# Kernel tuning notes

Measured on AMD Instinct MI355X. Metric: run time of the kernel, lower is better.

## Reference

```python
import jax, jax.numpy as jnp
import numpy as np

SEQ, B, I, H = 512, 64, 1024, 1024

def setup_inputs() -> dict:
    key = jax.random.key(0)
    ks = jax.random.split(key, 6)
    scale_ih = 1.0 / np.sqrt(I)
    scale_hh = 1.0 / np.sqrt(H)
    return {
        "input": jax.random.normal(ks[0], (SEQ, B, I), dtype=jnp.float32),
        "h_0": jax.random.normal(ks[1], (1, B, H), dtype=jnp.float32),
        "weight_ih": jax.random.normal(ks[2], (3 * H, I), dtype=jnp.float32) * scale_ih,
        "weight_hh": jax.random.normal(ks[3], (3 * H, H), dtype=jnp.float32) * scale_hh,
        "bias_ih": jax.random.normal(ks[4], (3 * H,), dtype=jnp.float32) * scale_hh,
        "bias_hh": jax.random.normal(ks[5], (3 * H,), dtype=jnp.float32) * scale_hh,
    }


def _gru_lbr0(input, h0, weight_ih, weight_hh, bias_ih, bias_hh):
    """Unidirectional GRU, ONNX linear_before_reset=0 semantics.

    r_t = sigmoid(x W_ir^T + b_ir + h W_hr^T + b_hr)
    z_t = sigmoid(x W_iz^T + b_iz + h W_hz^T + b_hz)
    n_t = tanh(x W_in^T + b_in + (r_t * h) W_hn^T + b_hn)
    h_t = (1 - z_t) * n_t + z_t * h
    """
    hidden = h0.shape[-1]
    # Precompute all input projections in one big GEMM: (S, B, 3H)
    gx = jnp.einsum('sbi,gi->sbg', input, weight_ih) + bias_ih
    W_hr, W_hz, W_hn = jnp.split(weight_hh, 3, axis=0)
    b_hr, b_hz, b_hn = jnp.split(bias_hh, 3, axis=0)

    def step(h, gx_t):
        gx_r, gx_z, gx_n = jnp.split(gx_t, 3, axis=-1)
        r = jax.nn.sigmoid(gx_r + h @ W_hr.T + b_hr)
        z = jax.nn.sigmoid(gx_z + h @ W_hz.T + b_hz)
        n = jnp.tanh(gx_n + (r * h) @ W_hn.T + b_hn)
        h_new = (1.0 - z) * n + z * h
        return h_new, h_new

    h_n, outputs = jax.lax.scan(step, h0, gx)
    return outputs, h_n  # (S, B, H), (B, H)


def reference(input, h_0, weight_ih, weight_hh, bias_ih, bias_hh):
    seq_len, batch, _ = input.shape
    hidden = weight_hh.shape[1]
    outputs, h_n = _gru_lbr0(input, h_0[0], weight_ih, weight_hh, bias_ih, bias_hh)
    # Match GRUWrapper output layout: Y = (S, num_dir=1, B, H), Y_h = (1, B, H)
    Y = outputs.reshape(seq_len, batch, 1, hidden).transpose(0, 2, 1, 3)
    Y_h = h_n[None, :, :]
    return (Y, Y_h)
```

## Files before the change

### kernel.cpp

```cpp
#include <hip/hip_runtime.h>

typedef unsigned short ushort_t;
typedef short sh8 __attribute__((ext_vector_type(8)));
typedef float f32x4 __attribute__((ext_vector_type(4)));

#define MFMA16(a,b,c) __builtin_amdgcn_mfma_f32_16x16x32_bf16((a),(b),(c),0,0,0)

#define SEQL   512
#define BATCH  64
#define HDIM   1024
#define G3     3072
#define AROWS  (SEQL*BATCH)
#define YSZ    (SEQL*BATCH*HDIM)
#define BH     (BATCH*HDIM)
#define NWG    64

__device__ __forceinline__ ushort_t f2bf(float x) {
  unsigned u = __float_as_uint(x);
  u += 0x7FFFu + ((u >> 16) & 1u);
  return (ushort_t)(u >> 16);
}
__device__ __forceinline__ float bf2f(ushort_t h) {
  return __uint_as_float(((unsigned)h) << 16);
}

__global__ void cvt_kernel(const float* __restrict__ wih, const float* __restrict__ h0,
                           ushort_t* __restrict__ WihH, ushort_t* __restrict__ WihL,
                           ushort_t* __restrict__ hH) {
  const int NW = G3 * HDIM;
  int i0 = blockIdx.x * blockDim.x + threadIdx.x;
  int stride = gridDim.x * blockDim.x;
  for (int i = i0; i < NW; i += stride) {
    float x = wih[i]; ushort_t h = f2bf(x);
    WihH[i] = h; WihL[i] = f2bf(x - bf2f(h));
  }
  for (int i = i0; i < BH; i += stride) {
    hH[i] = f2bf(h0[i]);
  }
}

__global__ __launch_bounds__(256) void gemm_gx(
    const float* __restrict__ A,
    const ushort_t* __restrict__ BHp, const ushort_t* __restrict__ BLp,
    const float* __restrict__ bias,
    float* __restrict__ gx)
{
  int bid = blockIdx.x;
  int mt = bid / 12, ntp = bid % 12;
  int w = threadIdx.x >> 6, l = threadIdx.x & 63;
  int lr = l & 15, lk = (l >> 4) * 8;

  f32x4 acc[2][2][8];
  #pragma unroll
  for (int n2 = 0; n2 < 2; ++n2)
    #pragma unroll
    for (int mi = 0; mi < 2; ++mi)
      #pragma unroll
      for (int ni = 0; ni < 8; ++ni) acc[n2][mi][ni] = (f32x4){0.f, 0.f, 0.f, 0.f};

  int arow0 = mt * 128 + w * 32 + lr;
  int brow0 = ntp * 256 + lr;

  for (int k0 = 0; k0 < HDIM; k0 += 32) {
    int ka = k0 + lk;
    sh8 aH[2], aL[2];
    #pragma unroll
    for (int mi = 0; mi < 2; ++mi) {
      const float* ap = A + (size_t)(arow0 + mi * 16) * HDIM + ka;
      float4 x0 = *(const float4*)ap;
      float4 x1 = *(const float4*)(ap + 4);
      float xs[8] = {x0.x, x0.y, x0.z, x0.w, x1.x, x1.y, x1.z, x1.w};
      #pragma unroll
      for (int j = 0; j < 8; ++j) {
        ushort_t h = f2bf(xs[j]);
        aH[mi][j] = (short)h;
        aL[mi][j] = (short)f2bf(xs[j] - bf2f(h));
      }
    }
    #pragma unroll
    for (int n2 = 0; n2 < 2; ++n2) {
      #pragma unroll
      for (int ni = 0; ni < 8; ++ni) {
        int brow = brow0 + n2 * 128 + ni * 16;
        const ushort_t* bh = BHp + (size_t)brow * HDIM + ka;
        const ushort_t* bl = BLp + (size_t)brow * HDIM + ka;
        sh8 bHf = *(const sh8*)bh;
        sh8 bLf = *(const sh8*)bl;
        #pragma unroll
        for (int mi = 0; mi < 2; ++mi) {
          acc[n2][mi][ni] = MFMA16(aH[mi], bHf, acc[n2][mi][ni]);
          acc[n2][mi][ni] = MFMA16(aH[mi], bLf, acc[n2][mi][ni]);
          acc[n2][mi][ni] = MFMA16(aL[mi], bHf, acc[n2][mi][ni]);
        }
      }
    }
  }
  int rb = (l >> 4) * 4;
  #pragma unroll
  for (int n2 = 0; n2 < 2; ++n2)
    #pragma unroll
    for (int mi = 0; mi < 2; ++mi)
      #pragma unroll
      for (int ni = 0; ni < 8; ++ni) {
        int col = ntp * 256 + n2 * 128 + ni * 16 + lr;
        float b = bias[col];
        #pragma unroll
        for (int j = 0; j < 4; ++j) {
          int row = mt * 128 + w * 32 + mi * 16 + rb + j;
          __builtin_nontemporal_store(acc[n2][mi][ni][j] + b, &gx[(size_t)row * G3 + col]);
        }
      }
}

__device__ __forceinline__ void gbar_flat(unsigned* slots, int g, int tid, unsigned e) {
  __syncthreads();
  if (tid < 64) {
    if (tid == 0)
      __hip_atomic_store(slots + g * 32, e, __ATOMIC_RELEASE, __HIP_MEMORY_SCOPE_AGENT);
    unsigned* sp = slots + tid * 32;
    while (__hip_atomic_load(sp, __ATOMIC_RELAXED, __HIP_MEMORY_SCOPE_AGENT) < e)
      __builtin_amdgcn_s_sleep(1);
    (void)__hip_atomic_load(sp, __ATOMIC_ACQUIRE, __HIP_MEMORY_SCOPE_AGENT);
  }
  __syncthreads();
}

__global__ __launch_bounds__(256, 1) void gru_rec(
    const float* __restrict__ gx,
    const float* __restrict__ whh,
    const float* __restrict__ bhh,
    const float* __restrict__ h0f,
    ushort_t* __restrict__ hH,
    ushort_t* __restrict__ rhH,
    float* __restrict__ Y, float* __restrict__ Yh,
    unsigned* __restrict__ slots)
{
  extern __shared__ char lds[];
  const int g = blockIdx.x;
  const int tid = threadIdx.x;
  const int w = tid >> 6, l = tid & 63;
  const int lr = l & 15, lk = (l >> 4) * 8, rb = (l >> 4) * 4;
  const int c0 = g * 16, m0 = w * 16;
  const int c = c0 + lr;

  #pragma unroll
  for (int p = 0; p < 32; ++p) {
    int q = tid + p * 256;
    int flat = q * 16;
    int lrow = flat >> 11;
    int off = flat & 2047;
    int dst = flat ^ ((lrow & 7) << 4);
    int col = off >> 1;
    const float* src;
    bool lo = false;
    if (lrow < 16)      src = whh + (size_t)(c0 + lrow) * HDIM + col;
    else if (lrow < 32) src = whh + (size_t)(1024 + c0 + lrow - 16) * HDIM + col;
    else if (lrow < 48) src = whh + (size_t)(2048 + c0 + lrow - 32) * HDIM + col;
    else              { src = whh + (size_t)(2048 + c0 + lrow - 48) * HDIM + col; lo = true; }
    float4 x0 = *(const float4*)src;
    float4 x1 = *(const float4*)(src + 4);
    float xs[8] = {x0.x, x0.y, x0.z, x0.w, x1.x, x1.y, x1.z, x1.w};
    union { ushort_t v[8]; sh8 s; } pk;
    #pragma unroll
    for (int j = 0; j < 8; ++j) {
      ushort_t hi = f2bf(xs[j]);
      pk.v[j] = lo ? f2bf(xs[j] - bf2f(hi)) : hi;
    }
    *(sh8*)(lds + dst) = pk.s;
  }
  __syncthreads();

  const float br = bhh[c], bz = bhh[1024 + c], bn = bhh[2048 + c];
  unsigned bar = 0;

  float hold[4];
  #pragma unroll
  for (int j = 0; j < 4; ++j) hold[j] = h0f[(m0 + rb + j) * HDIM + c];

  float gxr[4], gxz[4], gxn[4];
  #pragma unroll
  for (int j = 0; j < 4; ++j) {
    int b = m0 + rb + j;
    gxr[j] = __builtin_nontemporal_load(gx + (size_t)b * G3 + c);
    gxz[j] = __builtin_nontemporal_load(gx + (size_t)b * G3 + 1024 + c);
    gxn[j] = __builtin_nontemporal_load(gx + (size_t)b * G3 + 2048 + c);
  }

  for (int t = 0; t < SEQL; ++t) {
    const int par = t & 1;

    const ushort_t* ha = hH + par * BH + (size_t)(m0 + lr) * HDIM + lk;
    sh8 bufa[32];
    #pragma unroll
    for (int i = 0; i < 32; ++i) bufa[i] = *(const sh8*)(ha + i * 32);

    f32x4 accR = (f32x4){0,0,0,0}, accZ = (f32x4){0,0,0,0};
    #pragma unroll
    for (int i = 0; i < 32; ++i) {
      int byt = ((lr << 11) + ((i * 32 + lk) << 1)) ^ ((lr & 7) << 4);
      sh8 rW = *(const sh8*)(lds + byt);
      sh8 zW = *(const sh8*)(lds + 32768 + byt);
      accR = MFMA16(bufa[i], rW, accR);
      accZ = MFMA16(bufa[i], zW, accZ);
    }

    float zreg[4];
    #pragma unroll
    for (int j = 0; j < 4; ++j) {
      int b = m0 + rb + j;
      float pr = accR[j] + gxr[j] + br;
      float pz = accZ[j] + gxz[j] + bz;
      float r = 1.f / (1.f + __expf(-pr));
      zreg[j] = 1.f / (1.f + __expf(-pz));
      rhH[b * HDIM + c] = f2bf(r * hold[j]);
    }
    ++bar;
    gbar_flat(slots, g, tid, bar);

    const ushort_t* ra = rhH + (size_t)(m0 + lr) * HDIM + lk;
    #pragma unroll
    for (int i = 0; i < 32; ++i) bufa[i] = *(const sh8*)(ra + i * 32);

    int tn = (t + 1 < SEQL) ? t + 1 : t;
    {
      const float* gxn2 = gx + (size_t)tn * (BATCH * G3);
      #pragma unroll
      for (int j = 0; j < 4; ++j) {
        int b = m0 + rb + j;
        gxr[j] = __builtin_nontemporal_load(gxn2 + (size_t)b * G3 + c);
        gxz[j] = __builtin_nontemporal_load(gxn2 + (size_t)b * G3 + 1024 + c);
      }
    }

    f32x4 accN = (f32x4){0,0,0,0};
    #pragma unroll
    for (int i = 0; i < 32; ++i) {
      int byt = ((lr << 11) + ((i * 32 + lk) << 1)) ^ ((lr & 7) << 4);
      sh8 nW = *(const sh8*)(lds + 65536 + byt);
      sh8 nLo = *(const sh8*)(lds + 98304 + byt);
      accN = MFMA16(bufa[i], nW, accN);
      accN = MFMA16(bufa[i], nLo, accN);
    }

    ushort_t* hHn = hH + (par ^ 1) * BH;
    float gxnN[4];
    {
      const float* gxn2 = gx + (size_t)tn * (BATCH * G3);
      #pragma unroll
      for (int j = 0; j < 4; ++j) {
        int b = m0 + rb + j;
        gxnN[j] = __builtin_nontemporal_load(gxn2 + (size_t)b * G3 + 2048 + c);
      }
    }
    #pragma unroll
    for (int j = 0; j < 4; ++j) {
      int b = m0 + rb + j;
      float pn = accN[j] + gxn[j] + bn;
      float n = tanhf(pn);
      float z = zreg[j];
      float hnew = (1.f - z) * n + z * hold[j];
      hold[j] = hnew;
      __builtin_nontemporal_store(hnew, &Y[(size_t)t * BH + b * HDIM + c]);
      hHn[b * HDIM + c] = f2bf(hnew);
      if (t == SEQL - 1) __builtin_nontemporal_store(hnew, &Yh[b * HDIM + c]);
    }
    #pragma unroll
    for (int j = 0; j < 4; ++j) gxn[j] = gxnN[j];

    if (t < SEQL - 1) {
      ++bar;
      gbar_flat(slots, g, tid, bar);
    }
  }
}

extern "C" void kernel_launch(void* const* d_in, const int* in_sizes, int n_in,
                              void* d_out, int out_size, void* d_ws, size_t ws_size,
                              hipStream_t stream) {
  const float* input = (const float*)d_in[0];
  const float* h0    = (const float*)d_in[1];
  const float* wih   = (const float*)d_in[2];
  const float* whh   = (const float*)d_in[3];
  const float* bih   = (const float*)d_in[4];
  const float* bhh   = (const float*)d_in[5];

  char* ws = (char*)d_ws;
  size_t o = 0;
  float* gx = (float*)(ws + o);         o += (size_t)AROWS * G3 * 4;
  ushort_t* WihH = (ushort_t*)(ws + o); o += (size_t)G3 * HDIM * 2;
  ushort_t* WihL = (ushort_t*)(ws + o); o += (size_t)G3 * HDIM * 2;
  ushort_t* hH = (ushort_t*)(ws + o);   o += 2 * (size_t)BH * 2;
  ushort_t* rhH = (ushort_t*)(ws + o);  o += (size_t)BH * 2;
  unsigned* slots = (unsigned*)(ws + o); o += (size_t)NWG * 128;

  float* Y  = (float*)d_out;
  float* Yh = (float*)d_out + (size_t)YSZ;

  (void)hipFuncSetAttribute((const void*)gru_rec,
                            hipFuncAttributeMaxDynamicSharedMemorySize, 131072);

  (void)hipMemsetAsync(slots, 0, (size_t)NWG * 128, stream);
  cvt_kernel<<<2048, 256, 0, stream>>>(wih, h0, WihH, WihL, hH);
  gemm_gx<<<(AROWS / 128) * (G3 / 256), 256, 0, stream>>>(input, WihH, WihL, bih, gx);
  gru_rec<<<64, 256, 131072, stream>>>(gx, whh, bhh, h0, hH, rhH, Y, Yh, slots);
}
```

Before: 9.163 ms.

## Drop low-part activation MFMA and halve N tile in input-projection GEMM

Removes the aL (activation low-bf16) split so the input-projection GEMM does 2 MFMAs per tile instead of 3, skipping the xL*WH term. It also shrinks each block's N tile from 256 to 128 columns, doubling the grid and cutting accumulator registers. Fewer registers may raise occupancy, but the A tile is now converted twice as often across blocks. Accuracy drops because the input's low-order bits are lost, leaving only bf16 precision on x.

```diff
diff --git a/kernel.cpp b/kernel.cpp
--- a/kernel.cpp
+++ b/kernel.cpp
@@ -46,24 +46,22 @@
     float* __restrict__ gx)
 {
   int bid = blockIdx.x;
-  int mt = bid / 12, ntp = bid % 12;
+  int mt = bid / 24, nt = bid % 24;
   int w = threadIdx.x >> 6, l = threadIdx.x & 63;
   int lr = l & 15, lk = (l >> 4) * 8;
 
-  f32x4 acc[2][2][8];
-  #pragma unroll
-  for (int n2 = 0; n2 < 2; ++n2)
-    #pragma unroll
-    for (int mi = 0; mi < 2; ++mi)
-      #pragma unroll
-      for (int ni = 0; ni < 8; ++ni) acc[n2][mi][ni] = (f32x4){0.f, 0.f, 0.f, 0.f};
+  f32x4 acc[2][8];
+  #pragma unroll
+  for (int mi = 0; mi < 2; ++mi)
+    #pragma unroll
+    for (int ni = 0; ni < 8; ++ni) acc[mi][ni] = (f32x4){0.f, 0.f, 0.f, 0.f};
 
   int arow0 = mt * 128 + w * 32 + lr;
-  int brow0 = ntp * 256 + lr;
+  int brow0 = nt * 128 + lr;
 
   for (int k0 = 0; k0 < HDIM; k0 += 32) {
     int ka = k0 + lk;
-    sh8 aH[2], aL[2];
+    sh8 aH[2];
     #pragma unroll
     for (int mi = 0; mi < 2; ++mi) {
       const float* ap = A + (size_t)(arow0 + mi * 16) * HDIM + ka;
@@ -71,45 +69,34 @@
       float4 x1 = *(const float4*)(ap + 4);
       float xs[8] = {x0.x, x0.y, x0.z, x0.w, x1.x, x1.y, x1.z, x1.w};
       #pragma unroll
-      for (int j = 0; j < 8; ++j) {
-        ushort_t h = f2bf(xs[j]);
-        aH[mi][j] = (short)h;
-        aL[mi][j] = (short)f2bf(xs[j] - bf2f(h));
-      }
-    }
-    #pragma unroll
-    for (int n2 = 0; n2 < 2; ++n2) {
-      #pragma unroll
-      for (int ni = 0; ni < 8; ++ni) {
-        int brow = brow0 + n2 * 128 + ni * 16;
-        const ushort_t* bh = BHp + (size_t)brow * HDIM + ka;
-        const ushort_t* bl = BLp + (size_t)brow * HDIM + ka;
-        sh8 bHf = *(const sh8*)bh;
-        sh8 bLf = *(const sh8*)bl;
-        #pragma unroll
-        for (int mi = 0; mi < 2; ++mi) {
-          acc[n2][mi][ni] = MFMA16(aH[mi], bHf, acc[n2][mi][ni]);
-          acc[n2][mi][ni] = MFMA16(aH[mi], bLf, acc[n2][mi][ni]);
-          acc[n2][mi][ni] = MFMA16(aL[mi], bHf, acc[n2][mi][ni]);
-        }
+      for (int j = 0; j < 8; ++j) aH[mi][j] = (short)f2bf(xs[j]);
+    }
+    #pragma unroll
+    for (int ni = 0; ni < 8; ++ni) {
+      const ushort_t* bh = BHp + (size_t)(brow0 + ni * 16) * HDIM + ka;
+      const ushort_t* bl = BLp + (size_t)(brow0 + ni * 16) * HDIM + ka;
+      sh8 bHf = *(const sh8*)bh;
+      sh8 bLf = *(const sh8*)bl;
+      #pragma unroll
+      for (int mi = 0; mi < 2; ++mi) {
+        acc[mi][ni] = MFMA16(aH[mi], bHf, acc[mi][ni]);
+        acc[mi][ni] = MFMA16(aH[mi], bLf, acc[mi][ni]);
       }
     }
   }
   int rb = (l >> 4) * 4;
   #pragma unroll
-  for (int n2 = 0; n2 < 2; ++n2)
-    #pragma unroll
-    for (int mi = 0; mi < 2; ++mi)
-      #pragma unroll
-      for (int ni = 0; ni < 8; ++ni) {
-        int col = ntp * 256 + n2 * 128 + ni * 16 + lr;
-        float b = bias[col];
-        #pragma unroll
-        for (int j = 0; j < 4; ++j) {
-          int row = mt * 128 + w * 32 + mi * 16 + rb + j;
-          __builtin_nontemporal_store(acc[n2][mi][ni][j] + b, &gx[(size_t)row * G3 + col]);
-        }
-      }
+  for (int mi = 0; mi < 2; ++mi)
+    #pragma unroll
+    for (int ni = 0; ni < 8; ++ni) {
+      int col = nt * 128 + ni * 16 + lr;
+      float b = bias[col];
+      #pragma unroll
+      for (int j = 0; j < 4; ++j) {
+        int row = mt * 128 + w * 32 + mi * 16 + rb + j;
+        __builtin_nontemporal_store(acc[mi][ni][j] + b, &gx[(size_t)row * G3 + col]);
+      }
+    }
 }
 
 __device__ __forceinline__ void gbar_flat(unsigned* slots, int g, int tid, unsigned e) {
@@ -301,6 +288,6 @@
 
   (void)hipMemsetAsync(slots, 0, (size_t)NWG * 128, stream);
   cvt_kernel<<<2048, 256, 0, stream>>>(wih, h0, WihH, WihL, hH);
-  gemm_gx<<<(AROWS / 128) * (G3 / 256), 256, 0, stream>>>(input, WihH, WihL, bih, gx);
+  gemm_gx<<<(AROWS / 128) * (G3 / 128), 256, 0, stream>>>(input, WihH, WihL, bih, gx);
   gru_rec<<<64, 256, 131072, stream>>>(gx, whh, bhh, h0, hH, rhH, Y, Yh, slots);
 }
```

Measured after the change: 8.889 ms. -3.0%, faster.
